# Performance work log

Measured on AMD Instinct MI355X. Metric: run time of the kernel, lower is better.

## Reference

```python
import jax, jax.numpy as jnp
import numpy as np

EMBED = 3072
NQ = 32
NKV = 8
HD = EMBED // NQ  # 96
GROUPS = NQ // NKV  # 4
ROPE_BASE = 10000.0


def apply_rope(t, positions):
    # t: [b, h, s, d]; positions: [s] int
    d = t.shape[-1]
    inv_freq = 1.0 / (ROPE_BASE ** (jnp.arange(0, d, 2, dtype=jnp.float32) / d))  # [d/2]
    ang = positions.astype(jnp.float32)[:, None] * inv_freq[None, :]  # [s, d/2]
    cos = jnp.cos(ang)[None, None]  # [1,1,s,d/2]
    sin = jnp.sin(ang)[None, None]
    t1, t2 = t[..., : d // 2], t[..., d // 2 :]
    return jnp.concatenate([t1 * cos - t2 * sin, t2 * cos + t1 * sin], axis=-1)


def setup_inputs() -> dict:
    key = jax.random.key(0)
    k1, k2, k3 = jax.random.split(key, 3)
    b, s = 2, 2048
    x = jax.random.normal(k1, (b, s, EMBED), dtype=jnp.float32)
    positions = jnp.arange(s, dtype=jnp.int32)
    mask = jnp.triu(jnp.ones((s, s), dtype=bool), k=1)  # True = masked (causal)
    qkv_size = NQ * HD + 2 * NKV * HD  # 4608
    W_qkv = jax.random.normal(k2, (qkv_size, EMBED), dtype=jnp.float32) * (EMBED ** -0.5)
    W_o = jax.random.normal(k3, (EMBED, EMBED), dtype=jnp.float32) * (EMBED ** -0.5)
    return {"x": x, "positions": positions, "mask": mask, "W_qkv": W_qkv, "W_o": W_o}


def reference(x, positions, mask, W_qkv, W_o):
    b, s, _ = x.shape
    scaling = HD ** -0.5
    qkv = x @ W_qkv.T  # [b, s, 4608]
    q_size, kv_size = NQ * HD, NKV * HD
    q = qkv[..., :q_size].reshape(b, s, NQ, HD).transpose(0, 2, 1, 3)          # [b,NQ,s,d]
    k = qkv[..., q_size : q_size + kv_size].reshape(b, s, NKV, HD).transpose(0, 2, 1, 3)
    v = qkv[..., q_size + kv_size :].reshape(b, s, NKV, HD).transpose(0, 2, 1, 3)
    q = apply_rope(q, positions)
    k = apply_rope(k, positions)
    q = q.reshape(b, NKV, GROUPS, s, HD)
    scores = jnp.einsum("bkgsd,bktd->bkgst", q, k) * scaling  # [b,NKV,G,s,s]
    scores = jnp.where(mask[None, None, None], -jnp.inf, scores)
    attn = jax.nn.softmax(scores, axis=-1)
    out = jnp.einsum("bkgst,bktd->bkgsd", attn, v)
    out = out.reshape(b, NQ, s, HD).transpose(0, 2, 1, 3).reshape(b, s, NQ * HD)
    return out @ W_o.T
```

## Files before the change

### kernel.cpp

```cpp
#include <hip/hip_runtime.h>
#include <cstdint>

typedef unsigned short u16;
typedef unsigned int u32;
typedef __attribute__((ext_vector_type(4))) float f32x4;
typedef __attribute__((ext_vector_type(8))) __bf16 bf16x8;
typedef __attribute__((ext_vector_type(8))) unsigned short u16x8;
typedef __attribute__((ext_vector_type(4))) unsigned int u32x4;

#define S_LEN 2048
#define BATCH 2
#define NQH 32
#define NKVH 8
#define HD 96
#define EMB 3072
#define QKVN 4608
#define KOFF 3072
#define VOFF 3840

__device__ __forceinline__ u16 f2b(float f) {
    u32 u = __float_as_uint(f);
    u32 r = (u + 0x7fffu + ((u >> 16) & 1u)) >> 16;
    return (u16)r;
}
__device__ __forceinline__ float b2f(u16 h) { return __uint_as_float(((u32)h) << 16); }
__device__ __forceinline__ u32 cvtpk(float lo, float hi) {
    u32 r;
    asm("v_cvt_pk_bf16_f32 %0, %1, %2" : "=v"(r) : "v"(lo), "v"(hi));
    return r;
}

__global__ __launch_bounds__(256) void conv_f2b(const float* __restrict__ in,
                                                u16* __restrict__ outp, int n8) {
    const int i = blockIdx.x * 256 + threadIdx.x;
    if (i >= n8) return;
    const f32x4* q = (const f32x4*)(in + (size_t)i * 8);
    const f32x4 a = q[0], b = q[1];
    u16x8 t;
#pragma unroll
    for (int j = 0; j < 4; ++j) {
        t[j] = f2b(a[j]);
        t[j + 4] = f2b(b[j]);
    }
    *(u16x8*)(outp + (size_t)i * 8) = t;
}

typedef __attribute__((address_space(1))) const uint32_t gas_u32;
typedef __attribute__((address_space(3))) uint32_t las_u32;
__device__ __forceinline__ void gld_lds16(const u16* g, u16* l) {
    __builtin_amdgcn_global_load_lds((gas_u32*)g, (las_u32*)l, 16, 0, 0);
}

template <bool OUTF32>
__global__ __launch_bounds__(256) void gemm_bt(const u16* __restrict__ Ap,
                                               const u16* __restrict__ Bp,
                                               void* __restrict__ Cp,
                                               int M, int N, int K, int ldc) {
    __shared__ __align__(16) u16 As[128 * 32];
    __shared__ __align__(16) u16 Bs[128 * 32];
    const int tid = threadIdx.x;
    const int wave = tid >> 6, lane = tid & 63;
    const int bm = blockIdx.y * 128, bn = blockIdx.x * 128;
    const int wm = (wave >> 1) * 64, wn = (wave & 1) * 64;
    const int lrow = lane & 15, lk = (lane >> 4) * 8;
    const int ra = tid >> 2, ca = (tid & 3) * 8;

    const u16* gA0 = Ap + (size_t)(bm + ra) * K + ca;
    const u16* gA1 = Ap + (size_t)(bm + ra + 64) * K + ca;
    const u16* gB0 = Bp + (size_t)(bn + ra) * K + ca;
    const u16* gB1 = Bp + (size_t)(bn + ra + 64) * K + ca;
    u16* lA0 = As + (tid & 192) * 8;
    u16* lA1 = lA0 + 2048;
    u16* lB0 = Bs + (tid & 192) * 8;
    u16* lB1 = lB0 + 2048;

    f32x4 acc[4][4] = {};
    for (int k0 = 0; k0 < K; k0 += 32) {
        __syncthreads();
        gld_lds16(gA0 + k0, lA0);
        gld_lds16(gA1 + k0, lA1);
        gld_lds16(gB0 + k0, lB0);
        gld_lds16(gB1 + k0, lB1);
        __syncthreads();
        bf16x8 af[4], bfr[4];
#pragma unroll
        for (int mi = 0; mi < 4; ++mi)
            af[mi] = *(const bf16x8*)(As + (wm + mi * 16 + lrow) * 32 + lk);
#pragma unroll
        for (int ni = 0; ni < 4; ++ni)
            bfr[ni] = *(const bf16x8*)(Bs + (wn + ni * 16 + lrow) * 32 + lk);
#pragma unroll
        for (int mi = 0; mi < 4; ++mi)
#pragma unroll
            for (int ni = 0; ni < 4; ++ni)
                acc[mi][ni] = __builtin_amdgcn_mfma_f32_16x16x32_bf16(af[mi], bfr[ni],
                                                                      acc[mi][ni], 0, 0, 0);
    }
    const int orow = bm + wm + (lane >> 4) * 4;
    const int ocol = bn + wn + lrow;
#pragma unroll
    for (int mi = 0; mi < 4; ++mi)
#pragma unroll
        for (int ni = 0; ni < 4; ++ni)
#pragma unroll
            for (int r = 0; r < 4; ++r) {
                const size_t idx = (size_t)(orow + mi * 16 + r) * ldc + ocol + ni * 16;
                if constexpr (OUTF32)
                    ((float*)Cp)[idx] = acc[mi][ni][r];
                else
                    ((u16*)Cp)[idx] = f2b(acc[mi][ni][r]);
            }
}

__global__ __launch_bounds__(256) void gqa_rope(u16* __restrict__ qkv,
                                                const int* __restrict__ positions) {
    int i = blockIdx.x * 256 + threadIdx.x;
    const int pair = i % 48;
    int t = i / 48;
    const int head = t % (NQH + NKVH);
    const int bs = t / (NQH + NKVH);
    const int pos = positions[bs & (S_LEN - 1)];
    const size_t base = (size_t)bs * QKVN + (head < NQH ? head * HD : KOFF + (head - NQH) * HD);
    const float invf = __expf(-(float)(2 * pair) * (1.0f / 96.0f) * 9.210340371976184f);
    const float ang = (float)pos * invf;
    float sn, cs;
    __sincosf(ang, &sn, &cs);
    const float t1 = b2f(qkv[base + pair]);
    const float t2 = b2f(qkv[base + 48 + pair]);
    qkv[base + pair] = f2b(t1 * cs - t2 * sn);
    qkv[base + 48 + pair] = f2b(t2 * cs + t1 * sn);
}

__global__ __launch_bounds__(256) void gqa_attn3(const u16* __restrict__ qkv,
                                                 u16* __restrict__ out) {
    __shared__ __align__(16) u16 Ks[64 * 96];
    __shared__ __align__(16) u16 Vt[96 * 72];

    const int tid = threadIdx.x;
    const int wave = tid >> 6, lane = tid & 63;
    const int lrow = lane & 15, lhi = lane >> 4;
    const int bx = blockIdx.x;
    const int qt32 = 63 - (bx >> 4);
    const int kvh = (bx >> 1) & 7, bb = bx & 1;
    const int qh = kvh * 4 + wave;
    const int srow0 = bb * S_LEN + qt32 * 32;
    const int kb_last = (qt32 * 32 + 31) >> 6;
    const float cl2 = 0.10206207261596575f * 1.4426950408889634f;

    bf16x8 bq[2][3];
#pragma unroll
    for (int qt = 0; qt < 2; ++qt)
#pragma unroll
        for (int kd = 0; kd < 3; ++kd)
            bq[qt][kd] = *(const bf16x8*)(qkv + (size_t)(srow0 + qt * 16 + lrow) * QKVN +
                                          qh * 96 + kd * 32 + lhi * 8);

    float m_s[2] = {-3e38f, -3e38f}, l_s[2] = {0.0f, 0.0f};
    f32x4 oacc[6][2] = {};

    const int s0 = lrow + ((lane & 16) ? 32 : 0);
    const int s1 = s0 + 16;
    const bool khi = (lane & 32) != 0;

    const size_t kvrow0 = (size_t)(bb * S_LEN) * QKVN;
    for (int kb = 0; kb <= kb_last; ++kb) {
        __syncthreads();
        const size_t kbase = kvrow0 + (size_t)(kb * 64) * QKVN + KOFF + kvh * 96;
        const size_t vbase = kvrow0 + (size_t)(kb * 64) * QKVN + VOFF + kvh * 96;
        for (int u = tid; u < 768; u += 256) {
            const int oct = u % 12, row = u / 12;
            *(u16x8*)(Ks + row * 96 + oct * 8) =
                *(const u16x8*)(qkv + kbase + (size_t)row * QKVN + oct * 8);
        }
        for (int u = tid; u < 768; u += 256) {
            const int d = u % 96, so8 = u / 96;
            u16x8 v8;
#pragma unroll
            for (int j = 0; j < 8; ++j) v8[j] = qkv[vbase + (size_t)(so8 * 8 + j) * QKVN + d];
            *(u16x8*)(Vt + d * 72 + so8 * 8) = v8;
        }
        __syncthreads();

        bf16x8 ka[4][3];
#pragma unroll
        for (int kt = 0; kt < 4; ++kt)
#pragma unroll
            for (int kd = 0; kd < 3; ++kd)
                ka[kt][kd] = *(const bf16x8*)(Ks + (kt * 16 + lrow) * 96 + kd * 32 + lhi * 8);

        const int qoff = qt32 * 32 - kb * 64;
        const bool lastkb = (kb == kb_last);
        u32 bp[2][2][4];

#pragma unroll
        for (int qt = 0; qt < 2; ++qt) {
            const int qrelmax = qoff + qt * 16 + 15;
            f32x4 sacc[4] = {};
#pragma unroll
            for (int kt = 0; kt < 4; ++kt) {
                if (lastkb && kt * 16 > qrelmax) continue;
#pragma unroll
                for (int kd = 0; kd < 3; ++kd)
                    sacc[kt] = __builtin_amdgcn_mfma_f32_16x16x32_bf16(ka[kt][kd], bq[qt][kd],
                                                                       sacc[kt], 0, 0, 0);
            }
            float p[4][4];
            float mx = -3e38f;
            if (lastkb) {
                const int qrel = qoff + qt * 16 + lrow;
#pragma unroll
                for (int kt = 0; kt < 4; ++kt)
#pragma unroll
                    for (int r = 0; r < 4; ++r) {
                        const bool live = (kt * 16 + lhi * 4 + r) <= qrel;
                        const float s = live ? sacc[kt][r] : -3e38f;
                        p[kt][r] = s;
                        mx = fmaxf(mx, s);
                    }
            } else {
#pragma unroll
                for (int kt = 0; kt < 4; ++kt)
#pragma unroll
                    for (int r = 0; r < 4; ++r) {
                        p[kt][r] = sacc[kt][r];
                        mx = fmaxf(mx, sacc[kt][r]);
                    }
            }
            mx = fmaxf(mx, __shfl_xor(mx, 16));
            mx = fmaxf(mx, __shfl_xor(mx, 32));
            float mn = m_s[qt];
            if (!__all(mx - mn <= 20.0f)) {
                const float mnew = fmaxf(mn, mx);
                const float alpha = exp2f((mn - mnew) * cl2);
                m_s[qt] = mnew;
                mn = mnew;
                l_s[qt] *= alpha;
#pragma unroll
                for (int dt = 0; dt < 6; ++dt)
#pragma unroll
                    for (int r = 0; r < 4; ++r) oacc[dt][qt][r] *= alpha;
            }
            float rs = 0.0f;
#pragma unroll
            for (int kt = 0; kt < 4; ++kt)
#pragma unroll
                for (int r = 0; r < 4; ++r) {
                    const float pv = exp2f((p[kt][r] - mn) * cl2);
                    p[kt][r] = pv;
                    rs += pv;
                }
            rs += __shfl_xor(rs, 16);
            rs += __shfl_xor(rs, 32);
            l_s[qt] += rs;
            u32 pk[4][2];
#pragma unroll
            for (int kt = 0; kt < 4; ++kt) {
                pk[kt][0] = cvtpk(p[kt][0], p[kt][1]);
                pk[kt][1] = cvtpk(p[kt][2], p[kt][3]);
            }
#pragma unroll
            for (int kk = 0; kk < 2; ++kk) {
                const u32 a0 = (u32)__shfl((int)pk[kk * 2][0], s0, 64);
                const u32 b0 = (u32)__shfl((int)pk[kk * 2 + 1][0], s0, 64);
                const u32 a1 = (u32)__shfl((int)pk[kk * 2][1], s0, 64);
                const u32 b1 = (u32)__shfl((int)pk[kk * 2 + 1][1], s0, 64);
                const u32 a2 = (u32)__shfl((int)pk[kk * 2][0], s1, 64);
                const u32 b2 = (u32)__shfl((int)pk[kk * 2 + 1][0], s1, 64);
                const u32 a3 = (u32)__shfl((int)pk[kk * 2][1], s1, 64);
                const u32 b3 = (u32)__shfl((int)pk[kk * 2 + 1][1], s1, 64);
                bp[qt][kk][0] = khi ? b0 : a0;
                bp[qt][kk][1] = khi ? b1 : a1;
                bp[qt][kk][2] = khi ? b2 : a2;
                bp[qt][kk][3] = khi ? b3 : a3;
            }
        }

#pragma unroll
        for (int dt = 0; dt < 6; ++dt) {
            bf16x8 va[2];
#pragma unroll
            for (int kk = 0; kk < 2; ++kk)
                va[kk] = *(const bf16x8*)(Vt + (dt * 16 + lrow) * 72 + kk * 32 + lhi * 8);
#pragma unroll
            for (int qt = 0; qt < 2; ++qt)
#pragma unroll
                for (int kk = 0; kk < 2; ++kk) {
                    const u32x4 bv = {bp[qt][kk][0], bp[qt][kk][1], bp[qt][kk][2], bp[qt][kk][3]};
                    oacc[dt][qt] = __builtin_amdgcn_mfma_f32_16x16x32_bf16(
                        va[kk], __builtin_bit_cast(bf16x8, bv), oacc[dt][qt], 0, 0, 0);
                }
        }
    }

    const size_t obase = (size_t)srow0 * EMB + qh * 96;
#pragma unroll
    for (int qt = 0; qt < 2; ++qt) {
        const float inv = 1.0f / l_s[qt];
        const size_t rbase = obase + (size_t)(qt * 16 + lrow) * EMB;
#pragma unroll
        for (int dt = 0; dt < 6; ++dt)
#pragma unroll
            for (int rp = 0; rp < 2; ++rp) {
                const u32 pair = cvtpk(oacc[dt][qt][2 * rp] * inv, oacc[dt][qt][2 * rp + 1] * inv);
                *(u32*)(out + rbase + dt * 16 + lhi * 4 + 2 * rp) = pair;
            }
    }
}

extern "C" void kernel_launch(void* const* d_in, const int* in_sizes, int n_in,
                              void* d_out, int out_size, void* d_ws, size_t ws_size,
                              hipStream_t stream) {
    const float* x = (const float*)d_in[0];
    const int* positions = (const int*)d_in[1];
    const float* W_qkv = (const float*)d_in[3];
    const float* W_o = (const float*)d_in[4];
    float* out = (float*)d_out;

    const int M = BATCH * S_LEN;
    const size_t QKV_E = (size_t)M * QKVN;
    const size_t ATT_E = (size_t)M * EMB;
    const size_t X_E = (size_t)M * EMB;
    const size_t WQ_E = (size_t)EMB * EMB;
    const size_t WKV_E = (size_t)1536 * EMB;
    const size_t WO_E = (size_t)EMB * EMB;

    u16* qkv = (u16*)d_ws;
    u16* scratch = qkv + QKV_E;
    u16* xb = (u16*)d_out;

    conv_f2b<<<(int)(X_E / 8 / 256), 256, 0, stream>>>(x, xb, (int)(X_E / 8));

    conv_f2b<<<(int)(WKV_E / 8 / 256), 256, 0, stream>>>(W_qkv + (size_t)EMB * EMB, scratch,
                                                         (int)(WKV_E / 8));
    gemm_bt<false><<<dim3(1536 / 128, M / 128), 256, 0, stream>>>(xb, scratch, qkv + KOFF, M,
                                                                  1536, EMB, QKVN);

    conv_f2b<<<(int)(WQ_E / 8 / 256), 256, 0, stream>>>(W_qkv, scratch, (int)(WQ_E / 8));
    gemm_bt<false><<<dim3(EMB / 128, M / 128), 256, 0, stream>>>(xb, scratch, qkv, M, EMB, EMB,
                                                                 QKVN);

    gqa_rope<<<(BATCH * S_LEN * (NQH + NKVH) * 48) / 256, 256, 0, stream>>>(qkv, positions);

    gqa_attn3<<<dim3(1024), 256, 0, stream>>>(qkv, scratch);

    u16* wob = (u16*)d_ws;
    conv_f2b<<<(int)(WO_E / 8 / 256), 256, 0, stream>>>(W_o, wob, (int)(WO_E / 8));

    gemm_bt<true><<<dim3(EMB / 128, M / 128), 256, 0, stream>>>(scratch, wob, out, M, EMB, EMB,
                                                                EMB);
}
```

Baseline: 669.8 us.

## Double-buffer GEMM with async LDS prefetch, swizzle, and merge QKV projections

```diff
diff --git a/kernel.cpp b/kernel.cpp
--- a/kernel.cpp
+++ b/kernel.cpp
@@ -51,44 +51,147 @@
     __builtin_amdgcn_global_load_lds((gas_u32*)g, (las_u32*)l, 16, 0, 0);
 }
 
+#define WAITV4 asm volatile("s_waitcnt vmcnt(4)" ::: "memory")
+#define WAITV0 asm volatile("s_waitcnt vmcnt(0)" ::: "memory")
+#define BARRIER __builtin_amdgcn_s_barrier()
+#define SCHEDB __builtin_amdgcn_sched_barrier(0)
+
 template <bool OUTF32>
-__global__ __launch_bounds__(256) void gemm_bt(const u16* __restrict__ Ap,
-                                               const u16* __restrict__ Bp,
-                                               void* __restrict__ Cp,
-                                               int M, int N, int K, int ldc) {
-    __shared__ __align__(16) u16 As[128 * 32];
-    __shared__ __align__(16) u16 Bs[128 * 32];
+__global__ __launch_bounds__(256, 2) void gemm_bt_p(const u16* __restrict__ Ap,
+                                                    const u16* __restrict__ Bp,
+                                                    void* __restrict__ Cp,
+                                                    int M, int N, int K, int ldc) {
+    __shared__ __align__(16) u16 S[2 * 16384];
     const int tid = threadIdx.x;
     const int wave = tid >> 6, lane = tid & 63;
+    const int lrow = lane & 15, lhi = lane >> 4;
     const int bm = blockIdx.y * 128, bn = blockIdx.x * 128;
     const int wm = (wave >> 1) * 64, wn = (wave & 1) * 64;
-    const int lrow = lane & 15, lk = (lane >> 4) * 8;
-    const int ra = tid >> 2, ca = (tid & 3) * 8;
-
-    const u16* gA0 = Ap + (size_t)(bm + ra) * K + ca;
-    const u16* gA1 = Ap + (size_t)(bm + ra + 64) * K + ca;
-    const u16* gB0 = Bp + (size_t)(bn + ra) * K + ca;
-    const u16* gB1 = Bp + (size_t)(bn + ra + 64) * K + ca;
-    u16* lA0 = As + (tid & 192) * 8;
-    u16* lA1 = lA0 + 2048;
-    u16* lB0 = Bs + (tid & 192) * 8;
-    u16* lB1 = lB0 + 2048;
+    const int xsl = ((lhi ^ (lrow & 3) ^ ((lrow >> 2) & 3)) << 3);
+    const int srow = tid >> 2;
+    const int scol = (((tid & 3) ^ ((tid >> 2) & 3) ^ ((tid >> 4) & 3))) * 8;
+    const u16* gA0 = Ap + (size_t)(bm + srow) * K + scol;
+    const u16* gA1 = Ap + (size_t)(bm + 64 + srow) * K + scol;
+    const u16* gB0 = Bp + (size_t)(bn + srow) * K + scol;
+    const u16* gB1 = Bp + (size_t)(bn + 64 + srow) * K + scol;
+    u16* const dbase = S + (tid & 192) * 8;
 
     f32x4 acc[4][4] = {};
-    for (int k0 = 0; k0 < K; k0 += 32) {
-        __syncthreads();
-        gld_lds16(gA0 + k0, lA0);
-        gld_lds16(gA1 + k0, lA1);
-        gld_lds16(gB0 + k0, lB0);
-        gld_lds16(gB1 + k0, lB1);
-        __syncthreads();
+    const int nt = K >> 6;
+
+    gld_lds16(gA0, dbase);
+    gld_lds16(gA1, dbase + 2048);
+    gld_lds16(gB0, dbase + 8192);
+    gld_lds16(gB1, dbase + 8192 + 2048);
+    gld_lds16(gA0 + 32, dbase + 4096);
+    gld_lds16(gA1 + 32, dbase + 4096 + 2048);
+    gld_lds16(gB0 + 32, dbase + 8192 + 4096);
+    gld_lds16(gB1 + 32, dbase + 8192 + 4096 + 2048);
+
+    for (int t = 0; t + 1 < nt; ++t) {
+        const int cur = t & 1;
+        const u16* Ab = S + cur * 16384;
+        const u16* Bb = Ab + 8192;
+        u16* dn = dbase + (cur ^ 1) * 16384;
+        const int ko = (t + 1) << 6;
+
+        WAITV4;
+        BARRIER;
+        SCHEDB;
+        gld_lds16(gA0 + ko, dn);
+        gld_lds16(gA1 + ko, dn + 2048);
+        bf16x8 af[4], bf0[2], bf1[2];
+#pragma unroll
+        for (int mi = 0; mi < 4; ++mi)
+            af[mi] = *(const bf16x8*)(Ab + (wm + mi * 16 + lrow) * 32 + xsl);
+#pragma unroll
+        for (int ni = 0; ni < 2; ++ni)
+            bf0[ni] = *(const bf16x8*)(Bb + (wn + ni * 16 + lrow) * 32 + xsl);
+        __builtin_amdgcn_s_setprio(1);
+#pragma unroll
+        for (int mi = 0; mi < 4; ++mi)
+#pragma unroll
+            for (int ni = 0; ni < 2; ++ni)
+                acc[mi][ni] = __builtin_amdgcn_mfma_f32_16x16x32_bf16(af[mi], bf0[ni],
+                                                                      acc[mi][ni], 0, 0, 0);
+        __builtin_amdgcn_s_setprio(0);
+        gld_lds16(gB0 + ko, dn + 8192);
+        gld_lds16(gB1 + ko, dn + 8192 + 2048);
+#pragma unroll
+        for (int ni = 0; ni < 2; ++ni)
+            bf1[ni] = *(const bf16x8*)(Bb + (wn + (ni + 2) * 16 + lrow) * 32 + xsl);
+        __builtin_amdgcn_s_setprio(1);
+#pragma unroll
+        for (int mi = 0; mi < 4; ++mi)
+#pragma unroll
+            for (int ni = 0; ni < 2; ++ni)
+                acc[mi][ni + 2] = __builtin_amdgcn_mfma_f32_16x16x32_bf16(af[mi], bf1[ni],
+                                                                          acc[mi][ni + 2], 0, 0, 0);
+        __builtin_amdgcn_s_setprio(0);
+
+        WAITV4;
+        BARRIER;
+        SCHEDB;
+        gld_lds16(gA0 + ko + 32, dn + 4096);
+        gld_lds16(gA1 + ko + 32, dn + 4096 + 2048);
+#pragma unroll
+        for (int mi = 0; mi < 4; ++mi)
+            af[mi] = *(const bf16x8*)(Ab + 4096 + (wm + mi * 16 + lrow) * 32 + xsl);
+#pragma unroll
+        for (int ni = 0; ni < 2; ++ni)
+            bf0[ni] = *(const bf16x8*)(Bb + 4096 + (wn + ni * 16 + lrow) * 32 + xsl);
+        __builtin_amdgcn_s_setprio(1);
+#pragma unroll
+        for (int mi = 0; mi < 4; ++mi)
+#pragma unroll
+            for (int ni = 0; ni < 2; ++ni)
+                acc[mi][ni] = __builtin_amdgcn_mfma_f32_16x16x32_bf16(af[mi], bf0[ni],
+                                                                      acc[mi][ni], 0, 0, 0);
+        __builtin_amdgcn_s_setprio(0);
+        gld_lds16(gB0 + ko + 32, dn + 8192 + 4096);
+        gld_lds16(gB1 + ko + 32, dn + 8192 + 4096 + 2048);
+#pragma unroll
+        for (int ni = 0; ni < 2; ++ni)
+            bf1[ni] = *(const bf16x8*)(Bb + 4096 + (wn + (ni + 2) * 16 + lrow) * 32 + xsl);
+        __builtin_amdgcn_s_setprio(1);
+#pragma unroll
+        for (int mi = 0; mi < 4; ++mi)
+#pragma unroll
+            for (int ni = 0; ni < 2; ++ni)
+                acc[mi][ni + 2] = __builtin_amdgcn_mfma_f32_16x16x32_bf16(af[mi], bf1[ni],
+                                                                          acc[mi][ni + 2], 0, 0, 0);
+        __builtin_amdgcn_s_setprio(0);
+    }
+
+    {
+        const int cur = (nt - 1) & 1;
+        const u16* Ab = S + cur * 16384;
+        const u16* Bb = Ab + 8192;
+        WAITV4;
+        BARRIER;
+        SCHEDB;
         bf16x8 af[4], bfr[4];
 #pragma unroll
         for (int mi = 0; mi < 4; ++mi)
-            af[mi] = *(const bf16x8*)(As + (wm + mi * 16 + lrow) * 32 + lk);
+            af[mi] = *(const bf16x8*)(Ab + (wm + mi * 16 + lrow) * 32 + xsl);
 #pragma unroll
         for (int ni = 0; ni < 4; ++ni)
-            bfr[ni] = *(const bf16x8*)(Bs + (wn + ni * 16 + lrow) * 32 + lk);
+            bfr[ni] = *(const bf16x8*)(Bb + (wn + ni * 16 + lrow) * 32 + xsl);
+#pragma unroll
+        for (int mi = 0; mi < 4; ++mi)
+#pragma unroll
+            for (int ni = 0; ni < 4; ++ni)
+                acc[mi][ni] = __builtin_amdgcn_mfma_f32_16x16x32_bf16(af[mi], bfr[ni],
+                                                                      acc[mi][ni], 0, 0, 0);
+        WAITV0;
+        BARRIER;
+        SCHEDB;
+#pragma unroll
+        for (int mi = 0; mi < 4; ++mi)
+            af[mi] = *(const bf16x8*)(Ab + 4096 + (wm + mi * 16 + lrow) * 32 + xsl);
+#pragma unroll
+        for (int ni = 0; ni < 4; ++ni)
+            bfr[ni] = *(const bf16x8*)(Bb + 4096 + (wn + ni * 16 + lrow) * 32 + xsl);
 #pragma unroll
         for (int mi = 0; mi < 4; ++mi)
 #pragma unroll
@@ -96,7 +199,8 @@
                 acc[mi][ni] = __builtin_amdgcn_mfma_f32_16x16x32_bf16(af[mi], bfr[ni],
                                                                       acc[mi][ni], 0, 0, 0);
     }
-    const int orow = bm + wm + (lane >> 4) * 4;
+
+    const int orow = bm + wm + lhi * 4;
     const int ocol = bn + wn + lrow;
 #pragma unroll
     for (int mi = 0; mi < 4; ++mi)
@@ -320,32 +424,22 @@
     const size_t QKV_E = (size_t)M * QKVN;
     const size_t ATT_E = (size_t)M * EMB;
     const size_t X_E = (size_t)M * EMB;
-    const size_t WQ_E = (size_t)EMB * EMB;
-    const size_t WKV_E = (size_t)1536 * EMB;
+    const size_t WQKV_E = (size_t)QKVN * EMB;
     const size_t WO_E = (size_t)EMB * EMB;
 
     u16* qkv = (u16*)d_ws;
     u16* scratch = qkv + QKV_E;
-    u16* xb = (u16*)d_out;
+    u16* xb = scratch;
+    u16* wqkvb = (u16*)d_out;
+    u16* wob = (u16*)d_ws;
 
     conv_f2b<<<(int)(X_E / 8 / 256), 256, 0, stream>>>(x, xb, (int)(X_E / 8));
-
-    conv_f2b<<<(int)(WKV_E / 8 / 256), 256, 0, stream>>>(W_qkv + (size_t)EMB * EMB, scratch,
-                                                         (int)(WKV_E / 8));
-    gemm_bt<false><<<dim3(1536 / 128, M / 128), 256, 0, stream>>>(xb, scratch, qkv + KOFF, M,
-                                                                  1536, EMB, QKVN);
-
-    conv_f2b<<<(int)(WQ_E / 8 / 256), 256, 0, stream>>>(W_qkv, scratch, (int)(WQ_E / 8));
-    gemm_bt<false><<<dim3(EMB / 128, M / 128), 256, 0, stream>>>(xb, scratch, qkv, M, EMB, EMB,
-                                                                 QKVN);
-
+    conv_f2b<<<(int)(WQKV_E / 8 / 256), 256, 0, stream>>>(W_qkv, wqkvb, (int)(WQKV_E / 8));
+    gemm_bt_p<false>
+        <<<dim3(QKVN / 128, M / 128), 256, 0, stream>>>(xb, wqkvb, qkv, M, QKVN, EMB, QKVN);
     gqa_rope<<<(BATCH * S_LEN * (NQH + NKVH) * 48) / 256, 256, 0, stream>>>(qkv, positions);
-
     gqa_attn3<<<dim3(1024), 256, 0, stream>>>(qkv, scratch);
-
-    u16* wob = (u16*)d_ws;
     conv_f2b<<<(int)(WO_E / 8 / 256), 256, 0, stream>>>(W_o, wob, (int)(WO_E / 8));
-
-    gemm_bt<true><<<dim3(EMB / 128, M / 128), 256, 0, stream>>>(scratch, wob, out, M, EMB, EMB,
-                                                                EMB);
-}
+    gemm_bt_p<true>
+        <<<dim3(EMB / 128, M / 128), 256, 0, stream>>>(scratch, wob, out, M, EMB, EMB, EMB);
+}
```

Result: faster. 612.1 us (-8.6%).
